# Kernel optimization log

Measured on AMD Instinct MI355X. Metric: run time of the kernel, lower is better.

The kernel has to match this reference:

```python
import jax, jax.numpy as jnp
import numpy as np

B = 4
N1_PER = 16384  # fine points per scene
N2_PER = 4096   # coarse points per scene
IN_PLANES = 512
OUT_PLANES = 256
K = 3
CHUNK = 2048
BN_EPS = 1e-5


def _bn(x, g, b, m, v):
    # eval-mode BatchNorm1d: affine normalize with running stats
    return (x - m) * (g / jnp.sqrt(v + BN_EPS)) + b


def _interpolate_one(p1b, p2b, f2b):
    # p1b: [n1,3] queries, p2b: [n2,3] support, f2b: [n2,C]
    # k=3 inverse-distance weighted interpolation (pointops.interpolation)
    pq = p1b.reshape(-1, CHUNK, 3)  # chunk queries to avoid full [n1,n2] matrix

    def step(carry, q):  # q: [CHUNK,3]
        d2 = jnp.sum((q[:, None, :] - p2b[None, :, :]) ** 2, axis=-1)  # [CHUNK,n2]
        neg_d2, idx = jax.lax.top_k(-d2, K)                            # [CHUNK,K]
        dist = jnp.sqrt(jnp.maximum(-neg_d2, 1e-12))
        w = 1.0 / (dist + 1e-8)
        w = w / jnp.sum(w, axis=-1, keepdims=True)
        feat = f2b[idx]  # [CHUNK,K,C] gather
        return carry, jnp.einsum('qk,qkc->qc', w, feat)

    _, out = jax.lax.scan(step, None, pq)
    return out.reshape(-1, f2b.shape[-1])  # [n1,C]


def _forward(p1, x1, p2, x2, W1, b1, g1, be1, m1, v1, W2, b2, g2, be2, m2, v2):
    # branch 1: Linear-BN-ReLU on fine features
    h1 = jax.nn.relu(_bn(x1 @ W1.T + b1, g1, be1, m1, v1))  # [N1, out]
    # branch 2: Linear-BN-ReLU on coarse features, then kNN interpolation up
    h2 = jax.nn.relu(_bn(x2 @ W2.T + b2, g2, be2, m2, v2))  # [N2, out]
    # equal-sized scenes -> reshape + vmap over batch (offsets are [n,2n,...])
    p1b = p1.reshape(B, N1_PER, 3)
    p2b = p2.reshape(B, N2_PER, 3)
    h2b = h2.reshape(B, N2_PER, -1)
    up = jax.vmap(_interpolate_one)(p1b, p2b, h2b).reshape(-1, h2.shape[-1])
    return h1 + up


def setup_inputs() -> dict:
    key = jax.random.key(0)
    ks = jax.random.split(key, 16)
    p1 = jax.random.normal(ks[0], (B * N1_PER, 3), dtype=jnp.float32)
    x1 = jax.random.normal(ks[1], (B * N1_PER, OUT_PLANES), dtype=jnp.float32)
    p2 = jax.random.normal(ks[2], (B * N2_PER, 3), dtype=jnp.float32)
    x2 = jax.random.normal(ks[3], (B * N2_PER, IN_PLANES), dtype=jnp.float32)
    o1 = (jnp.arange(1, B + 1) * N1_PER).astype(jnp.int64)
    o2 = (jnp.arange(1, B + 1) * N2_PER).astype(jnp.int64)
    s1 = 1.0 / np.sqrt(OUT_PLANES)
    s2 = 1.0 / np.sqrt(IN_PLANES)
    W1 = jax.random.uniform(ks[4], (OUT_PLANES, OUT_PLANES), minval=-s1, maxval=s1)
    b1 = jax.random.uniform(ks[5], (OUT_PLANES,), minval=-s1, maxval=s1)
    W2 = jax.random.uniform(ks[6], (OUT_PLANES, IN_PLANES), minval=-s2, maxval=s2)
    b2 = jax.random.uniform(ks[7], (OUT_PLANES,), minval=-s2, maxval=s2)
    g1 = jnp.ones((OUT_PLANES,)); be1 = jnp.zeros((OUT_PLANES,))
    m1 = 0.1 * jax.random.normal(ks[8], (OUT_PLANES,))
    v1 = jax.random.uniform(ks[9], (OUT_PLANES,), minval=0.5, maxval=1.5)
    g2 = jnp.ones((OUT_PLANES,)); be2 = jnp.zeros((OUT_PLANES,))
    m2 = 0.1 * jax.random.normal(ks[10], (OUT_PLANES,))
    v2 = jax.random.uniform(ks[11], (OUT_PLANES,), minval=0.5, maxval=1.5)
    return dict(p1=p1, x1=x1, p2=p2, x2=x2, W1=W1, b1=b1, g1=g1, be1=be1,
                m1=m1, v1=v1, W2=W2, b2=b2, g2=g2, be2=be2, m2=m2, v2=v2,
                o1=o1, o2=o2)


def reference(p1, x1, p2, x2, W1, b1, g1, be1, m1, v1, W2, b2, g2, be2, m2, v2, o1, o2):
    return _forward(p1, x1, p2, x2, W1, b1, g1, be1, m1, v1, W2, b2, g2, be2, m2, v2)
```

## Files before the change

### kernel.cpp

```cpp
#include <hip/hip_runtime.h>

typedef __bf16 bf16x8 __attribute__((ext_vector_type(8)));
typedef float  f32x4  __attribute__((ext_vector_type(4)));
typedef float  f32x2  __attribute__((ext_vector_type(2)));

static __device__ __forceinline__ unsigned short f2bf(float f) {
  union { float f; unsigned int i; } c; c.f = f;
  unsigned int u = c.i;
  u += 0x7FFFu + ((u >> 16) & 1u);
  return (unsigned short)(u >> 16);
}

static __device__ __forceinline__ uint4 pk8(const float4 a, const float4 b) {
  uint4 o;
  o.x = ((unsigned int)f2bf(a.y) << 16) | f2bf(a.x);
  o.y = ((unsigned int)f2bf(a.w) << 16) | f2bf(a.z);
  o.z = ((unsigned int)f2bf(b.y) << 16) | f2bf(b.x);
  o.w = ((unsigned int)f2bf(b.w) << 16) | f2bf(b.z);
  return o;
}

static __device__ __forceinline__ bf16x8 pk8bf(const float4 a, const float4 b) {
  uint4 u = pk8(a, b);
  union { uint4 u; bf16x8 v; } c; c.u = u;
  return c.v;
}

#define WSEG0 65536u
#define WSEG1 196608u

__global__ __launch_bounds__(256) void cvt_w(const float* __restrict__ s0,
                                             const float* __restrict__ s1,
                                             unsigned short* __restrict__ dst) {
  const unsigned int e = (blockIdx.x * 256u + threadIdx.x) * 8u;
  const float* sp; unsigned int off;
  if (e < WSEG0) { sp = s0; off = e; }
  else           { sp = s1; off = e - WSEG0; }
  const float4* p = (const float4*)(sp + off);
  *(uint4*)(dst + e) = pk8(p[0], p[1]);
}

template<int K, bool FUSE>
__global__ __launch_bounds__(256) void gemm_wlds_k(
    const float* __restrict__ A,
    const unsigned short* __restrict__ Wm,
    const float* __restrict__ bias,
    const float* __restrict__ gam,
    const float* __restrict__ bet,
    const float* __restrict__ rmean,
    const float* __restrict__ rvar,
    float* __restrict__ outp,
    const float* __restrict__ h2f,
    const float* __restrict__ wgt,
    const int* __restrict__ idxg)
{
  constexpr int LDW = K + 8;
  __shared__ unsigned short WL[128][LDW];
  __shared__ float SC[128];
  __shared__ float SH[128];
  __shared__ float Wt[FUSE ? 128 * 3 : 1];
  __shared__ int   Id[FUSE ? 128 * 3 : 1];

  const int tid = threadIdx.x;
  const int bn = blockIdx.x;
  const int by = blockIdx.y;

  constexpr int CH = K / 8;
  for (int i = tid; i < 128 * CH; i += 256) {
    const int r = i / CH, c = (i % CH) * 8;
    *(uint4*)&WL[r][c] = *(const uint4*)(Wm + (size_t)(bn * 128 + r) * K + c);
  }
  if (tid < 128) {
    const int ch = bn * 128 + tid;
    const float sc = gam[ch] / sqrtf(rvar[ch] + 1e-5f);
    SC[tid] = sc;
    SH[tid] = (bias[ch] - rmean[ch]) * sc + bet[ch];
  }
  if (FUSE) {
    for (int i = tid; i < 128 * 3; i += 256) {
      Wt[i] = wgt[by * (128 * 3) + i];
      Id[i] = idxg[by * (128 * 3) + i];
    }
  }
  __syncthreads();

  const int wave = tid >> 6, lane = tid & 63;
  const int lr = lane & 15;
  const int kq = (lane >> 4) * 8;
  const int row0 = by * 128 + wave * 32;

  const float* Ap0 = A + (size_t)(row0 + lr) * K + kq;
  const float* Ap1 = A + (size_t)(row0 + 16 + lr) * K + kq;

  f32x4 acc[2][8];
  const f32x4 zero = {0.f, 0.f, 0.f, 0.f};
#pragma unroll
  for (int mi = 0; mi < 2; ++mi)
#pragma unroll
    for (int ni = 0; ni < 8; ++ni) acc[mi][ni] = zero;

#pragma unroll 4
  for (int kk = 0; kk < K; kk += 32) {
    const bf16x8 a0 = pk8bf(*(const float4*)(Ap0 + kk),
                            *(const float4*)(Ap0 + kk + 4));
    const bf16x8 a1 = pk8bf(*(const float4*)(Ap1 + kk),
                            *(const float4*)(Ap1 + kk + 4));
#pragma unroll
    for (int ni = 0; ni < 8; ++ni) {
      const bf16x8 bv = *(const bf16x8*)&WL[ni * 16 + lr][kk + kq];
      acc[0][ni] = __builtin_amdgcn_mfma_f32_16x16x32_bf16(a0, bv, acc[0][ni], 0, 0, 0);
      acc[1][ni] = __builtin_amdgcn_mfma_f32_16x16x32_bf16(a1, bv, acc[1][ni], 0, 0, 0);
    }
  }

#pragma unroll
  for (int mi = 0; mi < 2; ++mi) {
#pragma unroll
    for (int r = 0; r < 4; ++r) {
      const int rloc = wave * 32 + mi * 16 + (lane >> 4) * 4 + r;
      const size_t grow = (size_t)(by * 128 + rloc);
      float w0 = 0.f, w1 = 0.f, w2 = 0.f;
      const float *g0 = nullptr, *g1 = nullptr, *g2 = nullptr;
      if (FUSE) {
        w0 = Wt[rloc * 3 + 0]; w1 = Wt[rloc * 3 + 1]; w2 = Wt[rloc * 3 + 2];
        g0 = h2f + (size_t)Id[rloc * 3 + 0] * 256;
        g1 = h2f + (size_t)Id[rloc * 3 + 1] * 256;
        g2 = h2f + (size_t)Id[rloc * 3 + 2] * 256;
      }
#pragma unroll
      for (int ni = 0; ni < 8; ++ni) {
        const int cloc = ni * 16 + lr;
        const int gcol = bn * 128 + cloc;
        float v = acc[mi][ni][r] * SC[cloc] + SH[cloc];
        v = fmaxf(v, 0.f);
        if (FUSE) v += w0 * g0[gcol] + w1 * g1[gcol] + w2 * g2[gcol];
        outp[grow * 256 + gcol] = v;
      }
    }
  }
}

__global__ __launch_bounds__(256) void prep_pairs(const float* __restrict__ p2,
                                                  float* __restrict__ pp) {
  const int m = blockIdx.x * 256 + threadIdx.x;
  const float* s = p2 + m * 6;
  float* d = pp + m * 8;
  d[0] = s[0]; d[1] = s[3];
  d[2] = s[1]; d[3] = s[4];
  d[4] = s[2]; d[5] = s[5];
  d[6] = 0.f;  d[7] = 0.f;
}

__global__ __launch_bounds__(256) void knn_partial(const float* __restrict__ p1,
                                                   const float* __restrict__ ppair,
                                                   float* __restrict__ s_part,
                                                   int* __restrict__ i_part) {
#pragma clang fp contract(off)
  const int tid = threadIdx.x;
  const int qb = blockIdx.x, sp = blockIdx.y;
  const int scene = qb >> 6;
  const int pbase = scene * 4096 + sp * 512;
  const int qi = qb * 256 + tid;

  const float qx = p1[qi * 3 + 0];
  const float qy = p1[qi * 3 + 1];
  const float qz = p1[qi * 3 + 2];
  const f32x2 qxx = {qx, qx}, qyy = {qy, qy}, qzz = {qz, qz};

  float s0 = 1e30f, s1 = 1e30f, s2 = 1e30f;
  int i0 = pbase, i1 = pbase, i2 = pbase;

  const f32x2* pp = (const f32x2*)(ppair + (size_t)(pbase >> 1) * 8);
#pragma unroll 4
  for (int m = 0; m < 256; ++m) {
    const f32x2 X = pp[m * 4 + 0];
    const f32x2 Y = pp[m * 4 + 1];
    const f32x2 Z = pp[m * 4 + 2];
    const f32x2 dx = qxx - X;
    const f32x2 dy = qyy - Y;
    const f32x2 dz = qzz - Z;
    const f32x2 sv = (dx * dx + dy * dy) + dz * dz;
    const int jg = pbase + 2 * m;
    const float sa = sv.x, sb = sv.y;
    if (sa < s2) {
      if (sa < s1) {
        s2 = s1; i2 = i1;
        if (sa < s0) { s1 = s0; i1 = i0; s0 = sa; i0 = jg; }
        else         { s1 = sa; i1 = jg; }
      } else { s2 = sa; i2 = jg; }
    }
    if (sb < s2) {
      if (sb < s1) {
        s2 = s1; i2 = i1;
        if (sb < s0) { s1 = s0; i1 = i0; s0 = sb; i0 = jg + 1; }
        else         { s1 = sb; i1 = jg + 1; }
      } else { s2 = sb; i2 = jg + 1; }
    }
  }
  const int ob = (qi * 8 + sp) * 3;
  s_part[ob + 0] = s0; s_part[ob + 1] = s1; s_part[ob + 2] = s2;
  i_part[ob + 0] = i0; i_part[ob + 1] = i1; i_part[ob + 2] = i2;
}

__global__ __launch_bounds__(256) void knn_merge(const float* __restrict__ s_part,
                                                 const int* __restrict__ i_part,
                                                 float* __restrict__ wgt,
                                                 int* __restrict__ idxg) {
  const int qi = blockIdx.x * 256 + threadIdx.x;

  float s0 = 1e30f, s1 = 1e30f, s2 = 1e30f;
  int i0 = 0, i1 = 0, i2 = 0;
  const int base = qi * 24;
#pragma unroll
  for (int t = 0; t < 24; ++t) {
    const float s = s_part[base + t];
    const int id = i_part[base + t];
    if (s < s2) {
      if (s < s1) {
        s2 = s1; i2 = i1;
        if (s < s0) { s1 = s0; i1 = i0; s0 = s; i0 = id; }
        else        { s1 = s;  i1 = id; }
      } else { s2 = s; i2 = id; }
    }
  }
  const float d0 = sqrtf(fmaxf(s0, 1e-12f));
  const float d1 = sqrtf(fmaxf(s1, 1e-12f));
  const float d2 = sqrtf(fmaxf(s2, 1e-12f));
  float w0 = 1.f / (d0 + 1e-8f);
  float w1 = 1.f / (d1 + 1e-8f);
  float w2 = 1.f / (d2 + 1e-8f);
  const float inv = 1.f / (w0 + w1 + w2);
  wgt[qi * 3 + 0] = w0 * inv; wgt[qi * 3 + 1] = w1 * inv; wgt[qi * 3 + 2] = w2 * inv;
  idxg[qi * 3 + 0] = i0; idxg[qi * 3 + 1] = i1; idxg[qi * 3 + 2] = i2;
}

extern "C" void kernel_launch(void* const* d_in, const int* in_sizes, int n_in,
                              void* d_out, int out_size, void* d_ws, size_t ws_size,
                              hipStream_t stream) {
  const float* p1 = (const float*)d_in[0];
  const float* x1 = (const float*)d_in[1];
  const float* p2 = (const float*)d_in[2];
  const float* x2 = (const float*)d_in[3];
  const float* W1 = (const float*)d_in[4];
  const float* b1 = (const float*)d_in[5];
  const float* g1 = (const float*)d_in[6];
  const float* be1 = (const float*)d_in[7];
  const float* m1 = (const float*)d_in[8];
  const float* v1 = (const float*)d_in[9];
  const float* W2 = (const float*)d_in[10];
  const float* b2 = (const float*)d_in[11];
  const float* g2 = (const float*)d_in[12];
  const float* be2 = (const float*)d_in[13];
  const float* m2 = (const float*)d_in[14];
  const float* v2 = (const float*)d_in[15];

  char* ws = (char*)d_ws;
  unsigned short* W1b = (unsigned short*)ws;
  unsigned short* W2b = (unsigned short*)(ws + 131072);
  float* s_part = (float*)(ws + 1048576);
  int*   i_part = (int*)(ws + 7340032);
  float* h2f    = (float*)(ws + 16777216);
  float* ppair  = (float*)(ws + 33554432);
  float* wgt    = (float*)(ws + 33816576);
  int*   idxg   = (int*)(ws + 34603008);

  float* outp = (float*)d_out;

  cvt_w<<<96, 256, 0, stream>>>(W1, W2, W1b);

  gemm_wlds_k<512, false><<<dim3(2, 128), 256, 0, stream>>>(
      x2, W2b, b2, g2, be2, m2, v2, h2f, nullptr, nullptr, nullptr);

  prep_pairs<<<32, 256, 0, stream>>>(p2, ppair);

  knn_partial<<<dim3(256, 8), 256, 0, stream>>>(p1, ppair, s_part, i_part);

  knn_merge<<<256, 256, 0, stream>>>(s_part, i_part, wgt, idxg);

  gemm_wlds_k<256, true><<<dim3(2, 512), 256, 0, stream>>>(
      x1, W1b, b1, g1, be1, m1, v1, outp, h2f, wgt, idxg);
}
```

Before: 383.6 us.

## Stage weights through LDS in K-phases and shrink row tile for coarse GEMM

Instead of loading the block's whole weight slab (up to 128x520 bf16) into LDS at once, the GEMM now streams it in 128-wide K phases with a fixed small LDS buffer. This cuts LDS use so more blocks fit per CU (launch bounds request 4). The coarse x2 GEMM also uses 64 rows per block, doubling its grid. In exchange there are extra __syncthreads per phase and the weight loads are no longer overlapped with compute.

```diff
diff --git a/kernel.cpp b/kernel.cpp
--- a/kernel.cpp
+++ b/kernel.cpp
@@ -40,8 +40,8 @@
   *(uint4*)(dst + e) = pk8(p[0], p[1]);
 }
 
-template<int K, bool FUSE>
-__global__ __launch_bounds__(256) void gemm_wlds_k(
+template<int K, int RPB, bool FUSE>
+__global__ __launch_bounds__(256, 4) void gemm_ph(
     const float* __restrict__ A,
     const unsigned short* __restrict__ Wm,
     const float* __restrict__ bias,
@@ -54,22 +54,19 @@
     const float* __restrict__ wgt,
     const int* __restrict__ idxg)
 {
-  constexpr int LDW = K + 8;
+  constexpr int KS  = 128;
+  constexpr int LDW = KS + 8;
+  constexpr int MI  = RPB / 64;
   __shared__ unsigned short WL[128][LDW];
   __shared__ float SC[128];
   __shared__ float SH[128];
-  __shared__ float Wt[FUSE ? 128 * 3 : 1];
-  __shared__ int   Id[FUSE ? 128 * 3 : 1];
+  __shared__ float Wt[FUSE ? RPB * 3 : 1];
+  __shared__ int   Id[FUSE ? RPB * 3 : 1];
 
   const int tid = threadIdx.x;
   const int bn = blockIdx.x;
   const int by = blockIdx.y;
 
-  constexpr int CH = K / 8;
-  for (int i = tid; i < 128 * CH; i += 256) {
-    const int r = i / CH, c = (i % CH) * 8;
-    *(uint4*)&WL[r][c] = *(const uint4*)(Wm + (size_t)(bn * 128 + r) * K + c);
-  }
   if (tid < 128) {
     const int ch = bn * 128 + tid;
     const float sc = gam[ch] / sqrtf(rvar[ch] + 1e-5f);
@@ -77,48 +74,60 @@
     SH[tid] = (bias[ch] - rmean[ch]) * sc + bet[ch];
   }
   if (FUSE) {
-    for (int i = tid; i < 128 * 3; i += 256) {
-      Wt[i] = wgt[by * (128 * 3) + i];
-      Id[i] = idxg[by * (128 * 3) + i];
-    }
-  }
-  __syncthreads();
+    for (int i = tid; i < RPB * 3; i += 256) {
+      Wt[i] = wgt[by * (RPB * 3) + i];
+      Id[i] = idxg[by * (RPB * 3) + i];
+    }
+  }
 
   const int wave = tid >> 6, lane = tid & 63;
   const int lr = lane & 15;
   const int kq = (lane >> 4) * 8;
-  const int row0 = by * 128 + wave * 32;
-
-  const float* Ap0 = A + (size_t)(row0 + lr) * K + kq;
-  const float* Ap1 = A + (size_t)(row0 + 16 + lr) * K + kq;
-
-  f32x4 acc[2][8];
+  const int wrow0 = by * RPB + wave * (RPB / 4);
+
+  const float* Ap0 = A + (size_t)(wrow0 + lr) * K;
+  const float* Ap1 = A + (size_t)(wrow0 + 16 + lr) * K;
+
+  f32x4 acc[MI][8];
   const f32x4 zero = {0.f, 0.f, 0.f, 0.f};
 #pragma unroll
-  for (int mi = 0; mi < 2; ++mi)
+  for (int mi = 0; mi < MI; ++mi)
 #pragma unroll
     for (int ni = 0; ni < 8; ++ni) acc[mi][ni] = zero;
 
-#pragma unroll 4
-  for (int kk = 0; kk < K; kk += 32) {
-    const bf16x8 a0 = pk8bf(*(const float4*)(Ap0 + kk),
-                            *(const float4*)(Ap0 + kk + 4));
-    const bf16x8 a1 = pk8bf(*(const float4*)(Ap1 + kk),
-                            *(const float4*)(Ap1 + kk + 4));
-#pragma unroll
-    for (int ni = 0; ni < 8; ++ni) {
-      const bf16x8 bv = *(const bf16x8*)&WL[ni * 16 + lr][kk + kq];
-      acc[0][ni] = __builtin_amdgcn_mfma_f32_16x16x32_bf16(a0, bv, acc[0][ni], 0, 0, 0);
-      acc[1][ni] = __builtin_amdgcn_mfma_f32_16x16x32_bf16(a1, bv, acc[1][ni], 0, 0, 0);
-    }
-  }
-
-#pragma unroll
-  for (int mi = 0; mi < 2; ++mi) {
+  for (int ph = 0; ph < K / KS; ++ph) {
+    __syncthreads();
+#pragma unroll
+    for (int i = tid; i < 128 * (KS / 8); i += 256) {
+      const int r = i >> 4, g = i & 15;
+      *(uint4*)&WL[r][g * 8] =
+          *(const uint4*)(Wm + (size_t)(bn * 128 + r) * K + ph * KS + g * 8);
+    }
+    __syncthreads();
+#pragma unroll
+    for (int kk = 0; kk < KS; kk += 32) {
+      const int ka = ph * KS + kk + kq;
+      const bf16x8 a0 = pk8bf(*(const float4*)(Ap0 + ka),
+                              *(const float4*)(Ap0 + ka + 4));
+      bf16x8 a1;
+      if (MI == 2) a1 = pk8bf(*(const float4*)(Ap1 + ka),
+                              *(const float4*)(Ap1 + ka + 4));
+#pragma unroll
+      for (int ni = 0; ni < 8; ++ni) {
+        const bf16x8 bv = *(const bf16x8*)&WL[ni * 16 + lr][kk + kq];
+        acc[0][ni] = __builtin_amdgcn_mfma_f32_16x16x32_bf16(a0, bv, acc[0][ni], 0, 0, 0);
+        if (MI == 2)
+          acc[1][ni] = __builtin_amdgcn_mfma_f32_16x16x32_bf16(a1, bv, acc[1][ni], 0, 0, 0);
+      }
+    }
+  }
+
+#pragma unroll
+  for (int mi = 0; mi < MI; ++mi) {
 #pragma unroll
     for (int r = 0; r < 4; ++r) {
-      const int rloc = wave * 32 + mi * 16 + (lane >> 4) * 4 + r;
-      const size_t grow = (size_t)(by * 128 + rloc);
+      const int rloc = wave * (RPB / 4) + mi * 16 + (lane >> 4) * 4 + r;
+      const size_t grow = (size_t)(by * RPB + rloc);
       float w0 = 0.f, w1 = 0.f, w2 = 0.f;
       const float *g0 = nullptr, *g1 = nullptr, *g2 = nullptr;
       if (FUSE) {
@@ -268,7 +277,7 @@
 
   cvt_w<<<96, 256, 0, stream>>>(W1, W2, W1b);
 
-  gemm_wlds_k<512, false><<<dim3(2, 128), 256, 0, stream>>>(
+  gemm_ph<512, 64, false><<<dim3(2, 256), 256, 0, stream>>>(
       x2, W2b, b2, g2, be2, m2, v2, h2f, nullptr, nullptr, nullptr);
 
   prep_pairs<<<32, 256, 0, stream>>>(p2, ppair);
@@ -277,6 +286,6 @@
 
   knn_merge<<<256, 256, 0, stream>>>(s_part, i_part, wgt, idxg);
 
-  gemm_wlds_k<256, true><<<dim3(2, 512), 256, 0, stream>>>(
+  gemm_ph<256, 128, true><<<dim3(2, 512), 256, 0, stream>>>(
       x1, W1b, b1, g1, be1, m1, v1, outp, h2f, wgt, idxg);
 }
```

After: 352.9 us. -8.0%, faster.
